# Kernel optimization log

Measured on AMD Instinct MI355X. Metric: run time of the kernel, lower is better.

Reference implementation:

```python
import jax, jax.numpy as jnp
import numpy as np

TAU = 2.0      # LIF time constant
VTH = 1.0      # spike threshold
ALPHA = 4.0    # sigmoid surrogate slope (spikingjelly default)
EPS = 1e-5     # BN eps

@jax.custom_vjp
def spike_fn(x):
    return (x >= 0.0).astype(x.dtype)

def _spike_fwd(x):
    return spike_fn(x), x

def _spike_bwd(x, g):
    s = jax.nn.sigmoid(ALPHA * x)
    return (g * ALPHA * s * (1.0 - s),)

spike_fn.defvjp(_spike_fwd, _spike_bwd)

def conv2d(x, w, stride=1):
    return jax.lax.conv_general_dilated(
        x, w, (stride, stride), 'SAME',
        dimension_numbers=('NCHW', 'OIHW', 'NCHW'))

def bn(x, g, b, m, v):
    # eval-mode BatchNorm2d over channel axis 1
    scale = g / jnp.sqrt(v + EPS)
    return (x - m[:, None, None]) * scale[:, None, None] + b[:, None, None]

def lif_step(v, x):
    # charge, fire, hard reset to 0 (detach_reset)
    v = v + (x - v) / TAU
    s = spike_fn(v - VTH)
    v = (1.0 - jax.lax.stop_gradient(s)) * v
    return v, s

def lif_multistep(x_seq):
    v0 = jnp.zeros_like(x_seq[0])
    _, s = jax.lax.scan(lif_step, v0, x_seq)
    return s

def setup_inputs():
    key = jax.random.key(0)
    ks = jax.random.split(key, 8)
    T, B, C, H, W = 4, 4, 2, 128, 128
    E = 256
    x = jax.random.normal(ks[0], (T, B, C, H, W), jnp.float32)
    w_proj = jax.random.normal(ks[1], (E // 2, C, 3, 3), jnp.float32) * 0.2
    w_temp = jax.random.normal(ks[2], (C, E // 2, 3, 3), jnp.float32) * 0.05
    w1 = jax.random.normal(ks[3], (E, E // 2, 3, 3), jnp.float32) * 0.03
    w_res = jax.random.normal(ks[4], (E, E // 2, 1, 1), jnp.float32) * 0.09
    def bn_params(k, c):
        kk = jax.random.split(k, 2)
        return (jnp.abs(jax.random.normal(kk[0], (c,), jnp.float32)) + 0.5,
                jax.random.normal(kk[1], (c,), jnp.float32) * 0.1,
                jnp.zeros((c,), jnp.float32), jnp.ones((c,), jnp.float32))
    g0, b0, m0, v0 = bn_params(ks[5], E // 2)
    gt, bt, mt, vt = bn_params(ks[6], C)
    g1, b1, m1, v1 = bn_params(ks[7], E)
    gr, br, mr, vr = bn_params(jax.random.fold_in(key, 99), E)
    return dict(x=x, w_proj=w_proj, g0=g0, b0=b0, m0=m0, v0=v0,
                w_temp=w_temp, gt=gt, bt=bt, mt=mt, vt=vt,
                w1=w1, g1=g1, b1=b1, m1=m1, v1=v1,
                w_res=w_res, gr=gr, br=br, mr=mr, vr=vr)

def reference(x, w_proj, g0, b0, m0, v0, w_temp, gt, bt, mt, vt,
              w1, g1, b1, m1, v1, w_res, gr, br, mr, vr):
    T, B, C, H, W = x.shape
    half = w_proj.shape[0]
    # stf_1 recurrent coding: x_in[t] = x[t] + x_out[t-1]; LIF states persist
    def step(carry, x_t):
        x_out, vp, vtm = carry
        x_in = x_t + x_out
        h = bn(conv2d(x_in, w_proj), g0, b0, m0, v0)          # [B,half,H,W]
        vp, s1 = lif_step(vp, h)                              # proj_lif
        y = bn(conv2d(s1, w_temp), gt, bt, mt, vt)            # [B,C,H,W]
        vtm, s2 = lif_step(vtm, y)                            # proj_temporal_lif
        return (s2, vp, vtm), s1
    init = (jnp.zeros((B, C, H, W), x.dtype),
            jnp.zeros((B, half, H, W), x.dtype),
            jnp.zeros((B, C, H, W), x.dtype))
    _, spikes = jax.lax.scan(step, init, x)                   # [T,B,half,H,W]
    xf = spikes.reshape(T * B, half, H, W)
    xa = bn(conv2d(xf, w1), g1, b1, m1, v1).reshape(T, B, -1, H, W)
    xa = lif_multistep(xa)                                    # proj1_lif
    xr = bn(conv2d(xf, w_res), gr, br, mr, vr).reshape(T, B, -1, H, W)
    xr = lif_multistep(xr)                                    # proj_res_lif
    return xa + xr
```

## Files before the change

### kernel.cpp

```cpp
#include <hip/hip_runtime.h>
#include <math.h>

#define HW 16384

typedef __attribute__((ext_vector_type(8))) _Float16 half8;
typedef __attribute__((ext_vector_type(4))) float f32x4;

__global__ __launch_bounds__(256)
void k_reorder2(const float* __restrict__ w1, const float* __restrict__ wres,
                const float* __restrict__ g1, const float* __restrict__ b1,
                const float* __restrict__ m1, const float* __restrict__ v1,
                const float* __restrict__ gr, const float* __restrict__ br,
                const float* __restrict__ mr, const float* __restrict__ vr,
                short* __restrict__ whi, short* __restrict__ wmid,
                short* __restrict__ rhi, short* __restrict__ rmid,
                float* __restrict__ bias1, float* __restrict__ biasr) {
    int i = blockIdx.x * 256 + threadIdx.x;
    if (i < 294912) {
        int n = i / 1152, rem = i % 1152;
        int ic = rem / 9, tap = rem % 9;
        float sc = g1[n] / sqrtf(v1[n] + 1e-5f);
        float wv = (w1[i] * sc) * 4096.0f;
        _Float16 h = (_Float16)wv;
        float r1 = wv - (float)h;
        _Float16 m = (_Float16)r1;
        int kb = ic >> 5, q = (ic >> 3) & 3, j = ic & 7;
        size_t f = ((((size_t)(kb * 9 + tap)) * 4 + q) * 256 + n) * 8 + j;
        whi[f]  = __builtin_bit_cast(short, h);
        wmid[f] = __builtin_bit_cast(short, m);
    }
    if (i < 32768) {
        int n = i >> 7, ic = i & 127;
        float sc = gr[n] / sqrtf(vr[n] + 1e-5f);
        float wv = (wres[i] * sc) * 4096.0f;
        _Float16 h = (_Float16)wv;
        float r1 = wv - (float)h;
        _Float16 m = (_Float16)r1;
        int kb = ic >> 5, q = (ic >> 3) & 3, j = ic & 7;
        size_t f = (((size_t)kb * 4 + q) * 256 + n) * 8 + j;
        rhi[f]  = __builtin_bit_cast(short, h);
        rmid[f] = __builtin_bit_cast(short, m);
    }
    if (i < 256) {
        float sc1 = g1[i] / sqrtf(v1[i] + 1e-5f);
        bias1[i] = (b1[i] - m1[i] * sc1) * 4096.0f;
        float scr_ = gr[i] / sqrtf(vr[i] + 1e-5f);
        biasr[i] = (br[i] - mr[i] * scr_) * 4096.0f;
    }
}

__global__ __launch_bounds__(256)
void k_proj(const float* __restrict__ xt, const float* __restrict__ xout,
            const float* __restrict__ wp,
            const float* __restrict__ g, const float* __restrict__ bb,
            const float* __restrict__ mm, const float* __restrict__ vv,
            float* __restrict__ vp, unsigned char* __restrict__ s1t, int first) {
    __shared__ float xin[2 * 10 * 36];
    const int tid = threadIdx.x;
    const int b   = blockIdx.z >> 2;
    const int ocq = blockIdx.z & 3;
    const int gy0 = blockIdx.y * 8, gx0 = blockIdx.x * 32;

    for (int i = tid; i < 680; i += 256) {
        int ch = i / 340, rem = i % 340;
        int r = rem / 34, c = rem % 34;
        int gy = gy0 - 1 + r, gx = gx0 - 1 + c;
        float val = 0.f;
        if (gy >= 0 && gy < 128 && gx >= 0 && gx < 128) {
            int idx = ((b * 2 + ch) << 14) + (gy << 7) + gx;
            val = xt[idx];
            if (!first) val += xout[idx];
        }
        xin[(ch * 10 + r) * 36 + c] = val;
    }
    __syncthreads();

    const int prow = tid >> 5, pcol = tid & 31;
    float xw[2][3][3];
#pragma unroll
    for (int ch = 0; ch < 2; ++ch)
#pragma unroll
        for (int ky = 0; ky < 3; ++ky)
#pragma unroll
            for (int kx = 0; kx < 3; ++kx)
                xw[ch][ky][kx] = xin[(ch * 10 + prow + ky) * 36 + pcol + kx];

    const int pix = ((gy0 + prow) << 7) + gx0 + pcol;
    const int oc_beg = ocq * 32;
    unsigned int pk = 0u;
#pragma unroll
    for (int oo = 0; oo < 32; ++oo) {
        const int oc = oc_beg + oo;
        float acc = 0.f;
#pragma unroll
        for (int ch = 0; ch < 2; ++ch)
#pragma unroll
            for (int ky = 0; ky < 3; ++ky)
#pragma unroll
                for (int kx = 0; kx < 3; ++kx)
                    acc = fmaf(wp[((oc * 2 + ch) * 3 + ky) * 3 + kx], xw[ch][ky][kx], acc);
        float sc = g[oc] / sqrtf(vv[oc] + 1e-5f);
        float h  = (acc - mm[oc]) * sc + bb[oc];
        int idx = ((b * 128 + oc) << 14) + pix;
        float v = first ? 0.f : vp[idx];
        v = v + (h - v) * 0.5f;
        bool s = (v >= 1.0f);
        vp[idx] = s ? 0.f : v;
        pk |= (s ? 1u : 0u) << oo;
    }
    *(unsigned int*)(s1t + ((((size_t)b << 14) + pix) << 4) + ocq * 4) = pk;
}

__global__ __launch_bounds__(256)
void k_temp(const unsigned char* __restrict__ s1t, const float* __restrict__ wt,
            const float* __restrict__ g, const float* __restrict__ bb,
            const float* __restrict__ mm, const float* __restrict__ vv,
            float* __restrict__ vtm, float* __restrict__ xout, int first) {
    __shared__ unsigned char sl[49152];
    __shared__ float wls[2304];
    __shared__ float red[256];
    const int tid = threadIdx.x;
    const int b   = blockIdx.y;
    const int y0  = blockIdx.x;

    for (int i = tid; i < 2304; i += 256) wls[i] = wt[i];

    for (int i = tid; i < 384; i += 256) {
        int r = i >> 7, px = i & 127;
        int gy = y0 - 1 + r;
        uint4 d = make_uint4(0u, 0u, 0u, 0u);
        if (gy >= 0 && gy < 128)
            d = *(const uint4*)(s1t + ((((size_t)b << 14) + (gy << 7) + px) << 4));
        unsigned int bs[4] = {d.x, d.y, d.z, d.w};
#pragma unroll
        for (int icb = 0; icb < 16; ++icb) {
            unsigned int v8 = (bs[icb >> 2] >> ((icb & 3) * 8)) & 0xFFu;
            unsigned int lo = (v8 & 1u) | ((v8 & 2u) << 7) | ((v8 & 4u) << 14) | ((v8 & 8u) << 21);
            unsigned int hi = ((v8 >> 4) & 1u) | ((v8 & 32u) << 3) | ((v8 & 64u) << 10) | ((v8 & 128u) << 17);
            *(uint2*)&sl[(((icb * 3) + r) * 128 + (px ^ (icb & 7))) * 8] = make_uint2(lo, hi);
        }
    }
    __syncthreads();

    const int x = tid & 127, hf = tid >> 7;
    float a0 = 0.f, a1 = 0.f;
#pragma unroll 1
    for (int ii = 0; ii < 8; ++ii) {
        const int icb = hf * 8 + ii;
        int sw = icb & 7;
        const float* w0 = &wls[icb * 72];
        const float* w1_ = &wls[1152 + icb * 72];
#pragma unroll
        for (int dy = 0; dy < 3; ++dy) {
#pragma unroll
            for (int dx = 0; dx < 3; ++dx) {
                int xx = x - 1 + dx;
                if (xx < 0 || xx > 127) continue;
                uint2 d = *(const uint2*)&sl[((icb * 3 + dy) * 128 + (xx ^ sw)) * 8];
                int tap = dy * 3 + dx;
#pragma unroll
                for (int j = 0; j < 4; ++j) {
                    float f0 = (float)((d.x >> (8 * j)) & 0xFFu);
                    float f1 = (float)((d.y >> (8 * j)) & 0xFFu);
                    a0 = fmaf(w0[j * 9 + tap],        f0, a0);
                    a0 = fmaf(w0[(4 + j) * 9 + tap],  f1, a0);
                    a1 = fmaf(w1_[j * 9 + tap],       f0, a1);
                    a1 = fmaf(w1_[(4 + j) * 9 + tap], f1, a1);
                }
            }
        }
    }
    if (hf) { red[x] = a0; red[128 + x] = a1; }
    __syncthreads();
    if (!hf) {
        a0 += red[x]; a1 += red[128 + x];
#pragma unroll
        for (int oc = 0; oc < 2; ++oc) {
            float acc = (oc == 0) ? a0 : a1;
            float sc = g[oc] / sqrtf(vv[oc] + 1e-5f);
            float yv = (acc - mm[oc]) * sc + bb[oc];
            int idx = ((b * 2 + oc) << 14) + (y0 << 7) + x;
            float v = first ? 0.f : vtm[idx];
            v = v + (yv - v) * 0.5f;
            bool s = (v >= 1.0f);
            vtm[idx]  = s ? 0.f : v;
            xout[idx] = s ? 1.0f : 0.f;
        }
    }
}

__global__ __launch_bounds__(256, 3)
void k_fused(const unsigned char* __restrict__ s1c,
             const short* __restrict__ whi, const short* __restrict__ wmid,
             const short* __restrict__ rhi, const short* __restrict__ rmid,
             const float* __restrict__ bias1, const float* __restrict__ biasr,
             float* __restrict__ out) {
    __shared__ __align__(16) unsigned char bl[8704];
    __shared__ __align__(16) unsigned char xp[43520];

    const int tid = threadIdx.x;
    const int oc0 = blockIdx.x * 64;
    const int yb = blockIdx.y;
    const int b = yb >> 8, ry = (yb >> 2) & 63, cx = yb & 3;
    const int gy0 = ry * 2, gx0 = cx * 32;

    const int w   = tid >> 6, l = tid & 63;
    const int q   = l >> 4,  ln = l & 15;
    const int woc = w >> 1,  wpx = w & 1;

    const size_t wofs = ((size_t)q * 256 + oc0 + woc * 32 + ln) * 8;

    int pb[2], po[2], eb[2];
#pragma unroll
    for (int nt = 0; nt < 2; ++nt) {
        int px = wpx * 32 + nt * 16 + ln;
        int prow = px >> 5, pcol = px & 31;
        pb[nt] = prow * 34 + pcol;
        po[nt] = ((gy0 + prow) << 7) + gx0 + pcol;
        eb[nt] = pb[nt] * 80 + q * 16;
    }

    for (int cc = tid; cc < 544; cc += 256) {
        int t = cc / 136, p = cc - t * 136;
        int r = p / 34, c = p - r * 34;
        int gy = gy0 - 1 + r, gx = gx0 - 1 + c;
        uint4 d = make_uint4(0u, 0u, 0u, 0u);
        if (gy >= 0 && gy < 128 && gx >= 0 && gx < 128)
            d = *(const uint4*)(s1c + (size_t)t * 1048576 +
                                ((((size_t)b << 14) + (gy << 7) + gx) << 4));
        *(uint4*)(bl + cc * 16) = d;
    }
    __syncthreads();

    const float ds_ = 0.000244140625f;

    unsigned int srb[4];
    {
        f32x4 brr[2];
#pragma unroll
        for (int mt = 0; mt < 2; ++mt)
#pragma unroll
            for (int rg = 0; rg < 4; ++rg)
                brr[mt][rg] = biasr[oc0 + woc * 32 + mt * 16 + q * 4 + rg];

        float vres[2][2][4];
#pragma unroll
        for (int nt = 0; nt < 2; ++nt)
#pragma unroll
            for (int mt = 0; mt < 2; ++mt)
#pragma unroll
                for (int rg = 0; rg < 4; ++rg) vres[nt][mt][rg] = 0.f;

#pragma unroll
        for (int t = 0; t < 4; ++t) {
            const unsigned char* blt = bl + t * 2176;
            f32x4 accr[2][2];
#pragma unroll
            for (int nt = 0; nt < 2; ++nt)
#pragma unroll
                for (int mt = 0; mt < 2; ++mt) accr[nt][mt] = brr[mt];

#pragma unroll
            for (int kb = 0; kb < 4; ++kb) {
                half8 B4[2];
#pragma unroll
                for (int nt = 0; nt < 2; ++nt) {
                    unsigned int v8 = blt[(pb[nt] + 35) * 16 + kb * 4 + q];
                    uint4 pk;
                    pk.x = ((v8 & 1u)          | ((v8 & 2u)   << 15)) * 0x3C00u;
                    pk.y = (((v8 >> 2) & 1u)   | ((v8 & 8u)   << 13)) * 0x3C00u;
                    pk.z = (((v8 >> 4) & 1u)   | ((v8 & 32u)  << 11)) * 0x3C00u;
                    pk.w = (((v8 >> 6) & 1u)   | ((v8 & 128u) << 9 )) * 0x3C00u;
                    B4[nt] = __builtin_bit_cast(half8, pk);
                }
                half8 RH[2], RM[2];
#pragma unroll
                for (int mt = 0; mt < 2; ++mt) {
                    RH[mt] = *(const half8*)(rhi  + wofs + (size_t)kb * 8192 + mt * 128);
                    RM[mt] = *(const half8*)(rmid + wofs + (size_t)kb * 8192 + mt * 128);
                }
#pragma unroll
                for (int nt = 0; nt < 2; ++nt)
#pragma unroll
                    for (int mt = 0; mt < 2; ++mt) {
                        accr[nt][mt] = __builtin_amdgcn_mfma_f32_16x16x32_f16(RH[mt], B4[nt], accr[nt][mt], 0, 0, 0);
                        accr[nt][mt] = __builtin_amdgcn_mfma_f32_16x16x32_f16(RM[mt], B4[nt], accr[nt][mt], 0, 0, 0);
                    }
            }

            unsigned int sb = 0u;
#pragma unroll
            for (int nt = 0; nt < 2; ++nt)
#pragma unroll
                for (int mt = 0; mt < 2; ++mt)
#pragma unroll
                    for (int rg = 0; rg < 4; ++rg) {
                        float hr = accr[nt][mt][rg] * ds_;
                        float u = vres[nt][mt][rg];
                        u = u + (hr - u) * 0.5f;
                        bool sr_ = (u >= 1.0f);
                        vres[nt][mt][rg] = sr_ ? 0.f : u;
                        sb |= (sr_ ? 1u : 0u) << (mt * 8 + rg * 2 + nt);
                    }
            srb[t] = sb;
        }
    }

    f32x4 acc[4][2][2];
#pragma unroll
    for (int mt = 0; mt < 2; ++mt)
#pragma unroll
        for (int rg = 0; rg < 4; ++rg) {
            float bv = bias1[oc0 + woc * 32 + mt * 16 + q * 4 + rg];
#pragma unroll
            for (int t = 0; t < 4; ++t)
#pragma unroll
                for (int nt = 0; nt < 2; ++nt) acc[t][nt][mt][rg] = bv;
        }

    const short* bh = whi  + wofs;
    const short* bm = wmid + wofs;
#pragma unroll 1
    for (int kb = 0; kb < 4; ++kb) {
        if (kb) __syncthreads();
        for (int cc = tid; cc < 544; cc += 256) {
            unsigned int wd = *(const unsigned int*)(bl + cc * 16 + kb * 4);
            int t = cc / 136, p = cc - t * 136;
            unsigned char* dst = xp + t * 10880 + p * 80;
#pragma unroll
            for (int c2 = 0; c2 < 4; ++c2) {
                unsigned int x0 = wd >> (8 * c2);
                uint4 o;
                o.x = ((x0 & 1u)          | ((x0 & 2u)   << 15)) * 0x3C00u;
                o.y = (((x0 >> 2) & 1u)   | ((x0 & 8u)   << 13)) * 0x3C00u;
                o.z = (((x0 >> 4) & 1u)   | ((x0 & 32u)  << 11)) * 0x3C00u;
                o.w = (((x0 >> 6) & 1u)   | ((x0 & 128u) << 9 )) * 0x3C00u;
                *(uint4*)(dst + c2 * 16) = o;
            }
        }
        __syncthreads();

#pragma unroll
        for (int tap = 0; tap < 9; ++tap) {
            const int toff = ((tap / 3) * 34 + (tap % 3)) * 80;
            half8 AH[2], AM[2];
#pragma unroll
            for (int mt = 0; mt < 2; ++mt) {
                AH[mt] = *(const half8*)(bh + mt * 128);
                AM[mt] = *(const half8*)(bm + mt * 128);
            }
#pragma unroll
            for (int t = 0; t < 4; ++t) {
                half8 B4[2];
#pragma unroll
                for (int nt = 0; nt < 2; ++nt)
                    B4[nt] = *(const half8*)(xp + t * 10880 + eb[nt] + toff);
#pragma unroll
                for (int nt = 0; nt < 2; ++nt)
#pragma unroll
                    for (int mt = 0; mt < 2; ++mt) {
                        acc[t][nt][mt] = __builtin_amdgcn_mfma_f32_16x16x32_f16(AH[mt], B4[nt], acc[t][nt][mt], 0, 0, 0);
                        acc[t][nt][mt] = __builtin_amdgcn_mfma_f32_16x16x32_f16(AM[mt], B4[nt], acc[t][nt][mt], 0, 0, 0);
                    }
            }
            bh += 8192; bm += 8192;
        }
    }

    float va[2][2][4];
#pragma unroll
    for (int nt = 0; nt < 2; ++nt)
#pragma unroll
        for (int mt = 0; mt < 2; ++mt)
#pragma unroll
            for (int rg = 0; rg < 4; ++rg) va[nt][mt][rg] = 0.f;

#pragma unroll
    for (int t = 0; t < 4; ++t) {
        const size_t tb = ((size_t)((t * 4 + b) * 256 + oc0)) << 14;
#pragma unroll
        for (int mt = 0; mt < 2; ++mt)
#pragma unroll
            for (int rg = 0; rg < 4; ++rg) {
                const size_t ob = tb + ((size_t)(woc * 32 + mt * 16 + q * 4 + rg) << 14);
#pragma unroll
                for (int nt = 0; nt < 2; ++nt) {
                    float ha = acc[t][nt][mt][rg] * ds_;
                    float v = va[nt][mt][rg];
                    v = v + (ha - v) * 0.5f;
                    bool s = (v >= 1.0f);
                    va[nt][mt][rg] = s ? 0.f : v;
                    float sa = s ? 1.f : 0.f;
                    float sr = ((srb[t] >> (mt * 8 + rg * 2 + nt)) & 1u) ? 1.f : 0.f;
                    out[ob + po[nt]] = sa + sr;
                }
            }
    }
}

extern "C" void kernel_launch(void* const* d_in, const int* in_sizes, int n_in,
                              void* d_out, int out_size, void* d_ws, size_t ws_size,
                              hipStream_t stream) {
    const float* x      = (const float*)d_in[0];
    const float* w_proj = (const float*)d_in[1];
    const float* g0 = (const float*)d_in[2];
    const float* b0 = (const float*)d_in[3];
    const float* m0 = (const float*)d_in[4];
    const float* v0 = (const float*)d_in[5];
    const float* w_temp = (const float*)d_in[6];
    const float* gt = (const float*)d_in[7];
    const float* bt = (const float*)d_in[8];
    const float* mt = (const float*)d_in[9];
    const float* vt = (const float*)d_in[10];
    const float* w1 = (const float*)d_in[11];
    const float* g1 = (const float*)d_in[12];
    const float* b1 = (const float*)d_in[13];
    const float* m1 = (const float*)d_in[14];
    const float* v1 = (const float*)d_in[15];
    const float* w_res = (const float*)d_in[16];
    const float* gr = (const float*)d_in[17];
    const float* br = (const float*)d_in[18];
    const float* mr = (const float*)d_in[19];
    const float* vr = (const float*)d_in[20];

    char* ws = (char*)d_ws;
    unsigned char* s1c = (unsigned char*)ws;
    float* vp    = (float*)(ws + 4194304);
    float* vtm   = (float*)(ws + 37748736);
    float* xout  = (float*)(ws + 38273024);
    short* whi   = (short*)(ws + 38797312);
    short* wmid  = (short*)(ws + 39387136);
    short* rhi   = (short*)(ws + 39976960);
    short* rmid  = (short*)(ws + 40042496);
    float* bias1 = (float*)(ws + 40108032);
    float* biasr = (float*)(ws + 40109056);

    k_reorder2<<<dim3(1152), dim3(256), 0, stream>>>(
        w1, w_res, g1, b1, m1, v1, gr, br, mr, vr,
        whi, wmid, rhi, rmid, bias1, biasr);

    for (int t = 0; t < 4; ++t) {
        const float* xt = x + (size_t)t * 131072;
        unsigned char* s1t = s1c + (size_t)t * 1048576;
        k_proj<<<dim3(4, 16, 16), dim3(256), 0, stream>>>(
            xt, xout, w_proj, g0, b0, m0, v0, vp, s1t, t == 0);
        k_temp<<<dim3(128, 4), dim3(256), 0, stream>>>(
            s1t, w_temp, gt, bt, mt, vt, vtm, xout, t == 0);
    }

    k_fused<<<dim3(4, 1024), dim3(256), 0, stream>>>(
        s1c, whi, wmid, rhi, rmid, bias1, biasr, (float*)d_out);
}
```

Before: 630.3 us.

## Skip dead final LIF work, precompute BN scales, compact fused LDS layout

The last k_temp launch is dropped because its xout output is never consumed after the final timestep. Membrane-state writes are skipped on the last step that uses them. BN scale divisions and square roots are moved into the one-time reorder kernel. The k_fused LDS staging buffer loses its 80-byte per-pixel padding and drops to a 64-byte stride, with a flatter expansion loop, which reduces LDS footprint and may raise occupancy but can add bank conflicts.

```diff
diff --git a/kernel.cpp b/kernel.cpp
--- a/kernel.cpp
+++ b/kernel.cpp
@@ -12,9 +12,12 @@
                 const float* __restrict__ m1, const float* __restrict__ v1,
                 const float* __restrict__ gr, const float* __restrict__ br,
                 const float* __restrict__ mr, const float* __restrict__ vr,
+                const float* __restrict__ g0, const float* __restrict__ v0,
+                const float* __restrict__ gt, const float* __restrict__ vt,
                 short* __restrict__ whi, short* __restrict__ wmid,
                 short* __restrict__ rhi, short* __restrict__ rmid,
-                float* __restrict__ bias1, float* __restrict__ biasr) {
+                float* __restrict__ bias1, float* __restrict__ biasr,
+                float* __restrict__ psc, float* __restrict__ tsc) {
     int i = blockIdx.x * 256 + threadIdx.x;
     if (i < 294912) {
         int n = i / 1152, rem = i % 1152;
@@ -47,14 +50,17 @@
         float scr_ = gr[i] / sqrtf(vr[i] + 1e-5f);
         biasr[i] = (br[i] - mr[i] * scr_) * 4096.0f;
     }
+    if (i < 128) psc[i] = g0[i] / sqrtf(v0[i] + 1e-5f);
+    if (i < 2)   tsc[i] = gt[i] / sqrtf(vt[i] + 1e-5f);
 }
 
 __global__ __launch_bounds__(256)
 void k_proj(const float* __restrict__ xt, const float* __restrict__ xout,
             const float* __restrict__ wp,
-            const float* __restrict__ g, const float* __restrict__ bb,
-            const float* __restrict__ mm, const float* __restrict__ vv,
-            float* __restrict__ vp, unsigned char* __restrict__ s1t, int first) {
+            const float* __restrict__ psc, const float* __restrict__ bb,
+            const float* __restrict__ mm,
+            float* __restrict__ vp, unsigned char* __restrict__ s1t,
+            int first, int last) {
     __shared__ float xin[2 * 10 * 36];
     const int tid = threadIdx.x;
     const int b   = blockIdx.z >> 2;
@@ -99,13 +105,13 @@
 #pragma unroll
                 for (int kx = 0; kx < 3; ++kx)
                     acc = fmaf(wp[((oc * 2 + ch) * 3 + ky) * 3 + kx], xw[ch][ky][kx], acc);
-        float sc = g[oc] / sqrtf(vv[oc] + 1e-5f);
+        float sc = psc[oc];
         float h  = (acc - mm[oc]) * sc + bb[oc];
         int idx = ((b * 128 + oc) << 14) + pix;
         float v = first ? 0.f : vp[idx];
         v = v + (h - v) * 0.5f;
         bool s = (v >= 1.0f);
-        vp[idx] = s ? 0.f : v;
+        if (!last) vp[idx] = s ? 0.f : v;
         pk |= (s ? 1u : 0u) << oo;
     }
     *(unsigned int*)(s1t + ((((size_t)b << 14) + pix) << 4) + ocq * 4) = pk;
@@ -113,9 +119,10 @@
 
 __global__ __launch_bounds__(256)
 void k_temp(const unsigned char* __restrict__ s1t, const float* __restrict__ wt,
-            const float* __restrict__ g, const float* __restrict__ bb,
-            const float* __restrict__ mm, const float* __restrict__ vv,
-            float* __restrict__ vtm, float* __restrict__ xout, int first) {
+            const float* __restrict__ tsc, const float* __restrict__ bb,
+            const float* __restrict__ mm,
+            float* __restrict__ vtm, float* __restrict__ xout,
+            int first, int lastv) {
     __shared__ unsigned char sl[49152];
     __shared__ float wls[2304];
     __shared__ float red[256];
@@ -177,13 +184,13 @@
 #pragma unroll
         for (int oc = 0; oc < 2; ++oc) {
             float acc = (oc == 0) ? a0 : a1;
-            float sc = g[oc] / sqrtf(vv[oc] + 1e-5f);
+            float sc = tsc[oc];
             float yv = (acc - mm[oc]) * sc + bb[oc];
             int idx = ((b * 2 + oc) << 14) + (y0 << 7) + x;
             float v = first ? 0.f : vtm[idx];
             v = v + (yv - v) * 0.5f;
             bool s = (v >= 1.0f);
-            vtm[idx]  = s ? 0.f : v;
+            if (!lastv) vtm[idx] = s ? 0.f : v;
             xout[idx] = s ? 1.0f : 0.f;
         }
     }
@@ -196,7 +203,7 @@
              const float* __restrict__ bias1, const float* __restrict__ biasr,
              float* __restrict__ out) {
     __shared__ __align__(16) unsigned char bl[8704];
-    __shared__ __align__(16) unsigned char xp[43520];
+    __shared__ __align__(16) unsigned char xp[34816];
 
     const int tid = threadIdx.x;
     const int oc0 = blockIdx.x * 64;
@@ -217,7 +224,7 @@
         int prow = px >> 5, pcol = px & 31;
         pb[nt] = prow * 34 + pcol;
         po[nt] = ((gy0 + prow) << 7) + gx0 + pcol;
-        eb[nt] = pb[nt] * 80 + q * 16;
+        eb[nt] = pb[nt] * 64 + q * 16;
     }
 
     for (int cc = tid; cc < 544; cc += 256) {
@@ -323,26 +330,22 @@
 #pragma unroll 1
     for (int kb = 0; kb < 4; ++kb) {
         if (kb) __syncthreads();
-        for (int cc = tid; cc < 544; cc += 256) {
-            unsigned int wd = *(const unsigned int*)(bl + cc * 16 + kb * 4);
-            int t = cc / 136, p = cc - t * 136;
-            unsigned char* dst = xp + t * 10880 + p * 80;
-#pragma unroll
-            for (int c2 = 0; c2 < 4; ++c2) {
-                unsigned int x0 = wd >> (8 * c2);
-                uint4 o;
-                o.x = ((x0 & 1u)          | ((x0 & 2u)   << 15)) * 0x3C00u;
-                o.y = (((x0 >> 2) & 1u)   | ((x0 & 8u)   << 13)) * 0x3C00u;
-                o.z = (((x0 >> 4) & 1u)   | ((x0 & 32u)  << 11)) * 0x3C00u;
-                o.w = (((x0 >> 6) & 1u)   | ((x0 & 128u) << 9 )) * 0x3C00u;
-                *(uint4*)(dst + c2 * 16) = o;
-            }
+        for (int cc = tid; cc < 2176; cc += 256) {
+            int r = cc >> 2, c = cc & 3;
+            unsigned int dw = *(const unsigned int*)(bl + r * 16 + kb * 4);
+            unsigned int x0 = dw >> (c * 8);
+            uint4 o;
+            o.x = ((x0 & 1u)          | ((x0 & 2u)   << 15)) * 0x3C00u;
+            o.y = (((x0 >> 2) & 1u)   | ((x0 & 8u)   << 13)) * 0x3C00u;
+            o.z = (((x0 >> 4) & 1u)   | ((x0 & 32u)  << 11)) * 0x3C00u;
+            o.w = (((x0 >> 6) & 1u)   | ((x0 & 128u) << 9 )) * 0x3C00u;
+            *(uint4*)(xp + cc * 16) = o;
         }
         __syncthreads();
 
 #pragma unroll
         for (int tap = 0; tap < 9; ++tap) {
-            const int toff = ((tap / 3) * 34 + (tap % 3)) * 80;
+            const int toff = ((tap / 3) * 34 + (tap % 3)) * 64;
             half8 AH[2], AM[2];
 #pragma unroll
             for (int mt = 0; mt < 2; ++mt) {
@@ -354,7 +357,7 @@
                 half8 B4[2];
 #pragma unroll
                 for (int nt = 0; nt < 2; ++nt)
-                    B4[nt] = *(const half8*)(xp + t * 10880 + eb[nt] + toff);
+                    B4[nt] = *(const half8*)(xp + t * 8704 + eb[nt] + toff);
 #pragma unroll
                 for (int nt = 0; nt < 2; ++nt)
 #pragma unroll
@@ -434,18 +437,21 @@
     short* rmid  = (short*)(ws + 40042496);
     float* bias1 = (float*)(ws + 40108032);
     float* biasr = (float*)(ws + 40109056);
+    float* psc   = (float*)(ws + 40110080);
+    float* tsc   = (float*)(ws + 40110592);
 
     k_reorder2<<<dim3(1152), dim3(256), 0, stream>>>(
-        w1, w_res, g1, b1, m1, v1, gr, br, mr, vr,
-        whi, wmid, rhi, rmid, bias1, biasr);
+        w1, w_res, g1, b1, m1, v1, gr, br, mr, vr, g0, v0, gt, vt,
+        whi, wmid, rhi, rmid, bias1, biasr, psc, tsc);
 
     for (int t = 0; t < 4; ++t) {
         const float* xt = x + (size_t)t * 131072;
         unsigned char* s1t = s1c + (size_t)t * 1048576;
         k_proj<<<dim3(4, 16, 16), dim3(256), 0, stream>>>(
-            xt, xout, w_proj, g0, b0, m0, v0, vp, s1t, t == 0);
-        k_temp<<<dim3(128, 4), dim3(256), 0, stream>>>(
-            s1t, w_temp, gt, bt, mt, vt, vtm, xout, t == 0);
+            xt, xout, w_proj, psc, b0, m0, vp, s1t, t == 0, t == 3);
+        if (t < 3)
+            k_temp<<<dim3(128, 4), dim3(256), 0, stream>>>(
+                s1t, w_temp, tsc, bt, mt, vtm, xout, t == 0, t == 2);
     }
 
     k_fused<<<dim3(4, 1024), dim3(256), 0, stream>>>(
```

New measurement: 618.0 us. Within noise of the previous version (-1.9%).
